# Kernel optimization log

Measured on AMD Instinct MI355X. Metric: run time of the kernel, lower is better.

Reference implementation:

```python
import jax, jax.numpy as jnp
import numpy as np

HIDDEN = 1024
N_EXPERTS = 8
TOP_K = 2
INTER = 1408
N_SHARED = 2
SCALE = 1.0  # routed_scaling_factor


def setup_inputs() -> dict:
    key = jax.random.key(0)
    ks = jax.random.split(key, 9)
    s_h = 1.0 / np.sqrt(HIDDEN)
    s_i = 1.0 / np.sqrt(INTER)
    x = jax.random.normal(ks[0], (2, 2048, HIDDEN), dtype=jnp.float32)
    gate_w = jax.random.uniform(ks[1], (N_EXPERTS, HIDDEN), jnp.float32, -s_h, s_h)  # kaiming_uniform-ish
    # routed experts: SwiGLU (gate, up, down), stacked over experts
    wg = jax.random.uniform(ks[2], (N_EXPERTS, HIDDEN, INTER), jnp.float32, -s_h, s_h)
    wu = jax.random.uniform(ks[3], (N_EXPERTS, HIDDEN, INTER), jnp.float32, -s_h, s_h)
    wd = jax.random.uniform(ks[4], (N_EXPERTS, INTER, HIDDEN), jnp.float32, -s_i, s_i)
    # shared experts: one SwiGLU with intermediate = INTER * N_SHARED
    si = INTER * N_SHARED
    s_si = 1.0 / np.sqrt(si)
    swg = jax.random.uniform(ks[5], (HIDDEN, si), jnp.float32, -s_h, s_h)
    swu = jax.random.uniform(ks[6], (HIDDEN, si), jnp.float32, -s_h, s_h)
    swd = jax.random.uniform(ks[7], (si, HIDDEN), jnp.float32, -s_si, s_si)
    return {"x": x, "gate_w": gate_w, "wg": wg, "wu": wu, "wd": wd,
            "swg": swg, "swu": swu, "swd": swd}


def reference(x, gate_w, wg, wu, wd, swg, swu, swd):
    B, S, H = x.shape
    xf = x.reshape(-1, H)                              # [T, H]
    T = xf.shape[0]
    # --- MoEGate (fp32) ---
    logits = xf.astype(jnp.float32) @ gate_w.astype(jnp.float32).T   # [T, E]
    scores = jax.nn.softmax(logits, axis=-1)
    topw, topi = jax.lax.top_k(scores, TOP_K)          # [T, K]
    denom = topw.sum(axis=-1, keepdims=True) + 1e-20   # norm_topk_prob (top_k > 1)
    topw = topw / denom * SCALE
    # dense combine weights [T, E]: zero except at top-k expert slots
    wdense = jnp.zeros((T, N_EXPERTS), jnp.float32).at[
        jnp.arange(T)[:, None], topi].set(topw)
    # --- routed experts (SwiGLU), computed densely per expert and combined ---
    hg = jnp.einsum('th,ehi->eti', xf, wg)             # [E, T, I]
    hu = jnp.einsum('th,ehi->eti', xf, wu)             # [E, T, I]
    eo = jnp.einsum('eti,eih->eth', jax.nn.silu(hg) * hu, wd)   # [E, T, H]
    y = jnp.einsum('te,eth->th', wdense, eo)           # weighted scatter-combine
    # --- shared experts ---
    shared = (jax.nn.silu(xf @ swg) * (xf @ swu)) @ swd
    return (y + shared).reshape(B, S, H)
```

## Files before the change

kernel.cpp:

```cpp
#include <hip/hip_runtime.h>
#include <hip/hip_bf16.h>
#include <math.h>

#define HIDDEN 1024
#define NEXP 8
#define TOPK 2
#define INTER 1408
#define SINTER 2816
#define NTOK 4096
#define NROWS (NTOK * TOPK)
#define NPANEL 10
#define TROWS 16384
#define MAXT 136

typedef unsigned short ushort_t;
typedef __attribute__((ext_vector_type(8))) short short8;
typedef __attribute__((ext_vector_type(4))) float f32x4;

__device__ __forceinline__ ushort_t f2bf(float f) {
    unsigned int b = __float_as_uint(f);
    unsigned int r = (b + 0x7FFFu + ((b >> 16) & 1u)) >> 16;
    return (ushort_t)r;
}
__device__ __forceinline__ float bf2f(ushort_t u) {
    return __uint_as_float(((unsigned int)u) << 16);
}
__device__ __forceinline__ float silu_f(float g) {
    return g * (1.0f / (1.0f + __expf(-g)));
}
__device__ __forceinline__ int imin(int a, int b) { return a < b ? a : b; }

#define GLDS16(gp, lp) __builtin_amdgcn_global_load_lds(                     \
    (const __attribute__((address_space(1))) void*)(gp),                     \
    (__attribute__((address_space(3))) void*)(lp), 16, 0, 0)

__global__ void conv_x(const float* __restrict__ src, ushort_t* __restrict__ dst) {
    int i = (blockIdx.x * 256 + threadIdx.x) * 4;
    float4 v = *reinterpret_cast<const float4*>(&src[i]);
    union { ushort_t h[4]; unsigned long long ll; } p;
    p.h[0] = f2bf(v.x); p.h[1] = f2bf(v.y); p.h[2] = f2bf(v.z); p.h[3] = f2bf(v.w);
    *reinterpret_cast<unsigned long long*>(&dst[i]) = p.ll;
}

__global__ __launch_bounds__(256) void tconv64(const float* __restrict__ src,
                                               ushort_t* __restrict__ dst,
                                               int R, int C, long sstride,
                                               long dstride) {
    src += (size_t)blockIdx.z * sstride;
    dst += (size_t)blockIdx.z * dstride;
    __shared__ float tile[32][65];
    int ct = blockIdx.x * 32, rt = blockIdx.y * 64;
    int j = threadIdx.x;
    {
        int r = j >> 2;
        int c0 = (j & 3) * 8;
        const float* s = &src[(size_t)(rt + r) * C + ct + c0];
        float4 v0 = *reinterpret_cast<const float4*>(s);
        float4 v1 = *reinterpret_cast<const float4*>(s + 4);
        tile[c0 + 0][r] = v0.x; tile[c0 + 1][r] = v0.y;
        tile[c0 + 2][r] = v0.z; tile[c0 + 3][r] = v0.w;
        tile[c0 + 4][r] = v1.x; tile[c0 + 5][r] = v1.y;
        tile[c0 + 6][r] = v1.z; tile[c0 + 7][r] = v1.w;
    }
    __syncthreads();
    {
        int c = j >> 3;
        int r0 = (j & 7) * 8;
        union { ushort_t h[8]; short8 v; } p;
#pragma unroll
        for (int i = 0; i < 8; i++) p.h[i] = f2bf(tile[c][r0 + i]);
        *reinterpret_cast<short8*>(&dst[(size_t)(ct + c) * R + rt + r0]) = p.v;
    }
}

__global__ void gate_kernel(const float* __restrict__ x, const float* __restrict__ gw,
                            int* __restrict__ top_i, float* __restrict__ top_w) {
    int t = blockIdx.x;
    int lane = threadIdx.x;
    const float* xr = x + (size_t)t * HIDDEN;
    float acc[NEXP];
#pragma unroll
    for (int e = 0; e < NEXP; e++) acc[e] = 0.f;
    for (int j = 0; j < HIDDEN / 64; j++) {
        float xv = xr[lane + 64 * j];
#pragma unroll
        for (int e = 0; e < NEXP; e++)
            acc[e] = fmaf(xv, gw[e * HIDDEN + lane + 64 * j], acc[e]);
    }
#pragma unroll
    for (int e = 0; e < NEXP; e++) {
        float v = acc[e];
        for (int off = 32; off > 0; off >>= 1) v += __shfl_xor(v, off, 64);
        acc[e] = v;
    }
    if (lane == 0) {
        float mx = acc[0];
        for (int e = 1; e < NEXP; e++) mx = fmaxf(mx, acc[e]);
        float s[NEXP];
        float sum = 0.f;
        for (int e = 0; e < NEXP; e++) { s[e] = __expf(acc[e] - mx); sum += s[e]; }
        float inv = 1.0f / sum;
        for (int e = 0; e < NEXP; e++) s[e] *= inv;
        int e0 = 0;
        for (int e = 1; e < NEXP; e++) if (s[e] > s[e0]) e0 = e;
        int e1 = -1;
        for (int e = 0; e < NEXP; e++) {
            if (e == e0) continue;
            if (e1 < 0 || s[e] > s[e1]) e1 = e;
        }
        float w0 = s[e0], w1 = s[e1];
        float denom = w0 + w1 + 1e-20f;
        top_i[t * 2 + 0] = e0;
        top_i[t * 2 + 1] = e1;
        top_w[t * 2 + 0] = w0 / denom;
        top_w[t * 2 + 1] = w1 / denom;
    }
}

__global__ void assign_kernel(const int* __restrict__ top_i, int* __restrict__ cnt,
                              int* __restrict__ rnk) {
    int j = blockIdx.x * blockDim.x + threadIdx.x;
    if (j < NROWS) rnk[j] = atomicAdd(&cnt[top_i[j]], 1);
}

__global__ void scan_kernel(const int* __restrict__ cnt, int* __restrict__ offs2,
                            int* __restrict__ cnt2, int* __restrict__ task_pm) {
    if (threadIdx.x == 0) {
        int o = 0;
        for (int e = 0; e < NEXP; e++) { offs2[e] = o; cnt2[e] = cnt[e]; o += cnt[e]; }
        offs2[8] = NROWS;          cnt2[8] = NTOK;
        offs2[9] = NROWS + NTOK;   cnt2[9] = NTOK;
        offs2[10] = TROWS;
        int t = 0;
        for (int e = 0; e < NPANEL; e++)
            for (int m0 = 0; m0 < cnt2[e]; m0 += 128)
                task_pm[t++] = (e << 16) | (m0 >> 7);
        for (; t < MAXT; t++) task_pm[t] = -1;
    }
}

__global__ void fill_kernel(const int* __restrict__ top_i, const float* __restrict__ top_w,
                            const int* __restrict__ rnk, const int* __restrict__ offs2,
                            int* __restrict__ tok_of_row, float* __restrict__ w_of_row,
                            int* __restrict__ inv_row) {
    int j = blockIdx.x * blockDim.x + threadIdx.x;
    if (j < NROWS) {
        int row = offs2[top_i[j]] + rnk[j];
        tok_of_row[row] = j;
        w_of_row[row] = top_w[j];
        inv_row[j] = row;
    }
}

__global__ void fill_shared(int* __restrict__ tok_of_row) {
    int j = blockIdx.x * blockDim.x + threadIdx.x;
    tok_of_row[NROWS + j] = (j & (NTOK - 1)) << 1;
}

__global__ __launch_bounds__(256, 2) void gemm_gu(
    const ushort_t* __restrict__ xb, const ushort_t* __restrict__ WgT,
    const ushort_t* __restrict__ WuT, ushort_t* __restrict__ act,
    const int* __restrict__ tok_of_row, const int* __restrict__ offs2,
    const int* __restrict__ cnt2, const int* __restrict__ task_pm) {
    int T = gridDim.x;
    int orig = blockIdx.x;
    int logical = (orig & 7) * (T >> 3) + (orig >> 3);
    int task = logical % MAXT;
    int nidx = logical / MAXT;
    int tk = task_pm[task];
    if (tk < 0) return;
    int e = tk >> 16;
    int m0 = (tk & 0xffff) << 7;
    int mcnt = cnt2[e];
    int base = offs2[e];
    int n0 = nidx * 128;
    const ushort_t* Bg = WgT + (size_t)e * INTER * HIDDEN;
    const ushort_t* Bu = WuT + (size_t)e * INTER * HIDDEN;

    __shared__ short As[8 * 1024];
    __shared__ short Bgs[8 * 1024];
    __shared__ short Bus[8 * 1024];

    int tid = threadIdx.x;
    int wave = tid >> 6, lane = tid & 63;
    int wr = wave >> 1, wc = wave & 1;
    int lr = lane & 15;
    int kq = (lane >> 4) * 8;

    int r0 = m0 + 32 * wave + lr, r1 = r0 + 16;
    int rr0 = base + imin(r0, mcnt - 1);
    int rr1 = base + imin(r1, mcnt - 1);
    const ushort_t* srcA0 = xb + (size_t)(tok_of_row[rr0] >> 1) * HIDDEN + kq;
    const ushort_t* srcA1 = xb + (size_t)(tok_of_row[rr1] >> 1) * HIDDEN + kq;
    const ushort_t* srcBg0 = Bg + (size_t)(n0 + 32 * wave + lr) * HIDDEN + kq;
    const ushort_t* srcBg1 = srcBg0 + (size_t)16 * HIDDEN;
    const ushort_t* srcBu0 = Bu + (size_t)(n0 + 32 * wave + lr) * HIDDEN + kq;
    const ushort_t* srcBu1 = srcBu0 + (size_t)16 * HIDDEN;

    f32x4 accG[4][4] = {};
    f32x4 accU[4][4] = {};

    for (int k0 = 0; k0 < HIDDEN; k0 += 64) {
        GLDS16(srcA0 + k0,      &As[(2 * wave) * 1024]);
        GLDS16(srcA0 + k0 + 32, &As[(2 * wave) * 1024 + 512]);
        GLDS16(srcA1 + k0,      &As[(2 * wave + 1) * 1024]);
        GLDS16(srcA1 + k0 + 32, &As[(2 * wave + 1) * 1024 + 512]);
        GLDS16(srcBg0 + k0,      &Bgs[(2 * wave) * 1024]);
        GLDS16(srcBg0 + k0 + 32, &Bgs[(2 * wave) * 1024 + 512]);
        GLDS16(srcBg1 + k0,      &Bgs[(2 * wave + 1) * 1024]);
        GLDS16(srcBg1 + k0 + 32, &Bgs[(2 * wave + 1) * 1024 + 512]);
        GLDS16(srcBu0 + k0,      &Bus[(2 * wave) * 1024]);
        GLDS16(srcBu0 + k0 + 32, &Bus[(2 * wave) * 1024 + 512]);
        GLDS16(srcBu1 + k0,      &Bus[(2 * wave + 1) * 1024]);
        GLDS16(srcBu1 + k0 + 32, &Bus[(2 * wave + 1) * 1024 + 512]);
        __syncthreads();
#pragma unroll
        for (int s = 0; s < 2; s++) {
            short8 a[4], bg[4], bu[4];
#pragma unroll
            for (int mi = 0; mi < 4; mi++)
                a[mi] = *reinterpret_cast<const short8*>(
                    &As[(wr * 4 + mi) * 1024 + s * 512 + lane * 8]);
#pragma unroll
            for (int ni = 0; ni < 4; ni++) {
                bg[ni] = *reinterpret_cast<const short8*>(
                    &Bgs[(wc * 4 + ni) * 1024 + s * 512 + lane * 8]);
                bu[ni] = *reinterpret_cast<const short8*>(
                    &Bus[(wc * 4 + ni) * 1024 + s * 512 + lane * 8]);
            }
#pragma unroll
            for (int mi = 0; mi < 4; mi++)
#pragma unroll
                for (int ni = 0; ni < 4; ni++) {
                    accG[mi][ni] = __builtin_amdgcn_mfma_f32_16x16x32_bf16(
                        a[mi], bg[ni], accG[mi][ni], 0, 0, 0);
                    accU[mi][ni] = __builtin_amdgcn_mfma_f32_16x16x32_bf16(
                        a[mi], bu[ni], accU[mi][ni], 0, 0, 0);
                }
        }
        __syncthreads();
    }

#pragma unroll
    for (int mi = 0; mi < 4; mi++) {
#pragma unroll
        for (int r = 0; r < 4; r++) {
            int gm = m0 + wr * 64 + mi * 16 + (lane >> 4) * 4 + r;
            if (gm < mcnt) {
#pragma unroll
                for (int ni = 0; ni < 4; ni++) {
                    int col = n0 + wc * 64 + ni * 16 + lr;
                    float g = accG[mi][ni][r], u = accU[mi][ni][r];
                    act[(size_t)(base + gm) * INTER + col] = f2bf(silu_f(g) * u);
                }
            }
        }
    }
}

__global__ __launch_bounds__(256, 2) void gemm_down(
    const ushort_t* __restrict__ act, const ushort_t* __restrict__ WdT,
    ushort_t* __restrict__ part, const int* __restrict__ offs2,
    const int* __restrict__ cnt2, const int* __restrict__ task_pm) {
    int T = gridDim.x;
    int orig = blockIdx.x;
    int logical = (orig & 7) * (T >> 3) + (orig >> 3);
    int task = logical % MAXT;
    int nidx = logical / MAXT;
    int tk = task_pm[task];
    if (tk < 0) return;
    int e = tk >> 16;
    int m0 = (tk & 0xffff) << 7;
    int mcnt = cnt2[e];
    int base = offs2[e];
    int n0 = nidx * 256;
    const ushort_t* Bd = WdT + (size_t)e * HIDDEN * INTER;

    __shared__ short As[8 * 1024];
    __shared__ short Bs[16 * 1024];

    int tid = threadIdx.x;
    int wave = tid >> 6, lane = tid & 63;
    int wr = wave >> 1, wc = wave & 1;
    int lr = lane & 15;
    int kq = (lane >> 4) * 8;

    const ushort_t* srcA0 = act + (size_t)(base + m0 + 32 * wave + lr) * INTER + kq;
    const ushort_t* srcA1 = srcA0 + (size_t)16 * INTER;
    const ushort_t* srcB0 = Bd + (size_t)(n0 + 64 * wave + lr) * INTER + kq;
    const ushort_t* srcB1 = srcB0 + (size_t)16 * INTER;
    const ushort_t* srcB2 = srcB0 + (size_t)32 * INTER;
    const ushort_t* srcB3 = srcB0 + (size_t)48 * INTER;

    f32x4 acc[4][8] = {};

    for (int k0 = 0; k0 < INTER; k0 += 64) {
        GLDS16(srcA0 + k0,      &As[(2 * wave) * 1024]);
        GLDS16(srcA0 + k0 + 32, &As[(2 * wave) * 1024 + 512]);
        GLDS16(srcA1 + k0,      &As[(2 * wave + 1) * 1024]);
        GLDS16(srcA1 + k0 + 32, &As[(2 * wave + 1) * 1024 + 512]);
        GLDS16(srcB0 + k0,      &Bs[(4 * wave) * 1024]);
        GLDS16(srcB0 + k0 + 32, &Bs[(4 * wave) * 1024 + 512]);
        GLDS16(srcB1 + k0,      &Bs[(4 * wave + 1) * 1024]);
        GLDS16(srcB1 + k0 + 32, &Bs[(4 * wave + 1) * 1024 + 512]);
        GLDS16(srcB2 + k0,      &Bs[(4 * wave + 2) * 1024]);
        GLDS16(srcB2 + k0 + 32, &Bs[(4 * wave + 2) * 1024 + 512]);
        GLDS16(srcB3 + k0,      &Bs[(4 * wave + 3) * 1024]);
        GLDS16(srcB3 + k0 + 32, &Bs[(4 * wave + 3) * 1024 + 512]);
        __syncthreads();
#pragma unroll
        for (int s = 0; s < 2; s++) {
            short8 a[4], b[8];
#pragma unroll
            for (int mi = 0; mi < 4; mi++)
                a[mi] = *reinterpret_cast<const short8*>(
                    &As[(wr * 4 + mi) * 1024 + s * 512 + lane * 8]);
#pragma unroll
            for (int ni = 0; ni < 8; ni++)
                b[ni] = *reinterpret_cast<const short8*>(
                    &Bs[(wc * 8 + ni) * 1024 + s * 512 + lane * 8]);
#pragma unroll
            for (int mi = 0; mi < 4; mi++)
#pragma unroll
                for (int ni = 0; ni < 8; ni++)
                    acc[mi][ni] = __builtin_amdgcn_mfma_f32_16x16x32_bf16(
                        a[mi], b[ni], acc[mi][ni], 0, 0, 0);
        }
        __syncthreads();
    }

#pragma unroll
    for (int mi = 0; mi < 4; mi++) {
#pragma unroll
        for (int r = 0; r < 4; r++) {
            int gm = m0 + wr * 64 + mi * 16 + (lane >> 4) * 4 + r;
            if (gm < mcnt) {
#pragma unroll
                for (int ni = 0; ni < 8; ni++) {
                    int col = n0 + wc * 128 + ni * 16 + lr;
                    part[(size_t)(base + gm) * HIDDEN + col] = f2bf(acc[mi][ni][r]);
                }
            }
        }
    }
}

__global__ __launch_bounds__(256) void combine_kernel(
    const ushort_t* __restrict__ part, const int* __restrict__ inv_row,
    const float* __restrict__ w_of_row, float* __restrict__ out) {
    int t = blockIdx.x;
    int c = threadIdx.x * 4;
    int r0 = inv_row[2 * t], r1 = inv_row[2 * t + 1];
    float w0 = w_of_row[r0], w1 = w_of_row[r1];
    ushort4 a0 = *reinterpret_cast<const ushort4*>(&part[(size_t)r0 * HIDDEN + c]);
    ushort4 a1 = *reinterpret_cast<const ushort4*>(&part[(size_t)r1 * HIDDEN + c]);
    ushort4 a2 = *reinterpret_cast<const ushort4*>(&part[((size_t)NROWS + t) * HIDDEN + c]);
    ushort4 a3 = *reinterpret_cast<const ushort4*>(&part[((size_t)NROWS + NTOK + t) * HIDDEN + c]);
    float4 o;
    o.x = w0 * bf2f(a0.x) + w1 * bf2f(a1.x) + bf2f(a2.x) + bf2f(a3.x);
    o.y = w0 * bf2f(a0.y) + w1 * bf2f(a1.y) + bf2f(a2.y) + bf2f(a3.y);
    o.z = w0 * bf2f(a0.z) + w1 * bf2f(a1.z) + bf2f(a2.z) + bf2f(a3.z);
    o.w = w0 * bf2f(a0.w) + w1 * bf2f(a1.w) + bf2f(a2.w) + bf2f(a3.w);
    *reinterpret_cast<float4*>(&out[(size_t)t * HIDDEN + c]) = o;
}

extern "C" void kernel_launch(void* const* d_in, const int* in_sizes, int n_in,
                              void* d_out, int out_size, void* d_ws, size_t ws_size,
                              hipStream_t stream) {
    const float* x   = (const float*)d_in[0];
    const float* gw  = (const float*)d_in[1];
    const float* wg  = (const float*)d_in[2];
    const float* wu  = (const float*)d_in[3];
    const float* wd  = (const float*)d_in[4];
    const float* swg = (const float*)d_in[5];
    const float* swu = (const float*)d_in[6];
    const float* swd = (const float*)d_in[7];
    float* out = (float*)d_out;

    const size_t XB   = (size_t)NTOK * HIDDEN;
    const size_t WPAN = (size_t)NPANEL * INTER * HIDDEN;
    const size_t ACT  = (size_t)TROWS * INTER;
    const size_t PART = (size_t)TROWS * HIDDEN;
    ushort_t* xb   = (ushort_t*)d_ws;
    ushort_t* wgT  = xb + XB;
    ushort_t* wuT  = wgT + WPAN;
    ushort_t* wdT  = wuT + WPAN;
    ushort_t* act  = wdT + WPAN;
    ushort_t* part = act + ACT;
    int* ib = (int*)(part + PART);
    int* top_i      = ib;
    int* rnk        = ib + NROWS;
    int* cnt        = ib + 2 * NROWS;
    int* offs2      = ib + 2 * NROWS + 8;
    int* cnt2       = offs2 + 16;
    int* task_pm    = cnt2 + 16;
    int* tok_of_row = task_pm + MAXT;
    int* inv_row    = tok_of_row + TROWS;
    float* top_w    = (float*)(inv_row + NROWS);
    float* w_of_row = top_w + NROWS;

    conv_x<<<(NTOK * HIDDEN) / (256 * 4), 256, 0, stream>>>(x, xb);
    tconv64<<<dim3(INTER / 32, HIDDEN / 64, NEXP), 256, 0, stream>>>(
        wg, wgT, HIDDEN, INTER, (long)HIDDEN * INTER, (long)INTER * HIDDEN);
    tconv64<<<dim3(INTER / 32, HIDDEN / 64, NEXP), 256, 0, stream>>>(
        wu, wuT, HIDDEN, INTER, (long)HIDDEN * INTER, (long)INTER * HIDDEN);
    tconv64<<<dim3(SINTER / 32, HIDDEN / 64, 1), 256, 0, stream>>>(
        swg, wgT + (size_t)8 * INTER * HIDDEN, HIDDEN, SINTER, 0, 0);
    tconv64<<<dim3(SINTER / 32, HIDDEN / 64, 1), 256, 0, stream>>>(
        swu, wuT + (size_t)8 * INTER * HIDDEN, HIDDEN, SINTER, 0, 0);
    tconv64<<<dim3(HIDDEN / 32, INTER / 64, NEXP), 256, 0, stream>>>(
        wd, wdT, INTER, HIDDEN, (long)INTER * HIDDEN, (long)HIDDEN * INTER);
    tconv64<<<dim3(HIDDEN / 32, INTER / 64, 2), 256, 0, stream>>>(
        swd, wdT + (size_t)8 * HIDDEN * INTER, INTER, HIDDEN,
        (long)INTER * HIDDEN, (long)HIDDEN * INTER);

    gate_kernel<<<NTOK, 64, 0, stream>>>(x, gw, top_i, top_w);
    hipMemsetAsync(cnt, 0, 8 * sizeof(int), stream);
    assign_kernel<<<NROWS / 256, 256, 0, stream>>>(top_i, cnt, rnk);
    scan_kernel<<<1, 1, 0, stream>>>(cnt, offs2, cnt2, task_pm);
    fill_kernel<<<NROWS / 256, 256, 0, stream>>>(top_i, top_w, rnk, offs2,
                                                 tok_of_row, w_of_row, inv_row);
    fill_shared<<<NROWS / 256, 256, 0, stream>>>(tok_of_row);

    gemm_gu<<<MAXT * (INTER / 128), 256, 0, stream>>>(
        xb, wgT, wuT, act, tok_of_row, offs2, cnt2, task_pm);
    gemm_down<<<MAXT * (HIDDEN / 256), 256, 0, stream>>>(
        act, wdT, part, offs2, cnt2, task_pm);
    combine_kernel<<<NTOK, 256, 0, stream>>>(part, inv_row, w_of_row, out);
}
```

Before: 390.4 us.

## Double-buffer LDS tiles in expert GEMMs to overlap loads with MFMA

```diff
diff --git a/kernel.cpp b/kernel.cpp
--- a/kernel.cpp
+++ b/kernel.cpp
@@ -177,9 +177,9 @@
     const ushort_t* Bg = WgT + (size_t)e * INTER * HIDDEN;
     const ushort_t* Bu = WuT + (size_t)e * INTER * HIDDEN;
 
-    __shared__ short As[8 * 1024];
-    __shared__ short Bgs[8 * 1024];
-    __shared__ short Bus[8 * 1024];
+    __shared__ short As[2][8 * 512];
+    __shared__ short Bgs[2][8 * 512];
+    __shared__ short Bus[2][8 * 512];
 
     int tid = threadIdx.x;
     int wave = tid >> 6, lane = tid & 63;
@@ -200,46 +200,49 @@
     f32x4 accG[4][4] = {};
     f32x4 accU[4][4] = {};
 
-    for (int k0 = 0; k0 < HIDDEN; k0 += 64) {
-        GLDS16(srcA0 + k0,      &As[(2 * wave) * 1024]);
-        GLDS16(srcA0 + k0 + 32, &As[(2 * wave) * 1024 + 512]);
-        GLDS16(srcA1 + k0,      &As[(2 * wave + 1) * 1024]);
-        GLDS16(srcA1 + k0 + 32, &As[(2 * wave + 1) * 1024 + 512]);
-        GLDS16(srcBg0 + k0,      &Bgs[(2 * wave) * 1024]);
-        GLDS16(srcBg0 + k0 + 32, &Bgs[(2 * wave) * 1024 + 512]);
-        GLDS16(srcBg1 + k0,      &Bgs[(2 * wave + 1) * 1024]);
-        GLDS16(srcBg1 + k0 + 32, &Bgs[(2 * wave + 1) * 1024 + 512]);
-        GLDS16(srcBu0 + k0,      &Bus[(2 * wave) * 1024]);
-        GLDS16(srcBu0 + k0 + 32, &Bus[(2 * wave) * 1024 + 512]);
-        GLDS16(srcBu1 + k0,      &Bus[(2 * wave + 1) * 1024]);
-        GLDS16(srcBu1 + k0 + 32, &Bus[(2 * wave + 1) * 1024 + 512]);
-        __syncthreads();
-#pragma unroll
-        for (int s = 0; s < 2; s++) {
-            short8 a[4], bg[4], bu[4];
-#pragma unroll
-            for (int mi = 0; mi < 4; mi++)
-                a[mi] = *reinterpret_cast<const short8*>(
-                    &As[(wr * 4 + mi) * 1024 + s * 512 + lane * 8]);
+#define STAGE_GU(buf, k0)                                                    \
+    do {                                                                     \
+        GLDS16(srcA0 + (k0), &As[buf][(2 * wave) * 512]);                    \
+        GLDS16(srcA1 + (k0), &As[buf][(2 * wave + 1) * 512]);                \
+        GLDS16(srcBg0 + (k0), &Bgs[buf][(2 * wave) * 512]);                  \
+        GLDS16(srcBg1 + (k0), &Bgs[buf][(2 * wave + 1) * 512]);              \
+        GLDS16(srcBu0 + (k0), &Bus[buf][(2 * wave) * 512]);                  \
+        GLDS16(srcBu1 + (k0), &Bus[buf][(2 * wave + 1) * 512]);              \
+    } while (0)
+
+    STAGE_GU(0, 0);
+    asm volatile("s_waitcnt vmcnt(0)" ::: "memory");
+    __builtin_amdgcn_s_barrier();
+
+    const int NT = HIDDEN / 32;
+    for (int t = 0; t < NT; t++) {
+        int cur = t & 1;
+        if (t + 1 < NT) STAGE_GU(cur ^ 1, (t + 1) * 32);
+        short8 a[4], bg[4], bu[4];
+#pragma unroll
+        for (int mi = 0; mi < 4; mi++)
+            a[mi] = *reinterpret_cast<const short8*>(
+                &As[cur][(wr * 4 + mi) * 512 + lane * 8]);
+#pragma unroll
+        for (int ni = 0; ni < 4; ni++) {
+            bg[ni] = *reinterpret_cast<const short8*>(
+                &Bgs[cur][(wc * 4 + ni) * 512 + lane * 8]);
+            bu[ni] = *reinterpret_cast<const short8*>(
+                &Bus[cur][(wc * 4 + ni) * 512 + lane * 8]);
+        }
+#pragma unroll
+        for (int mi = 0; mi < 4; mi++)
 #pragma unroll
             for (int ni = 0; ni < 4; ni++) {
-                bg[ni] = *reinterpret_cast<const short8*>(
-                    &Bgs[(wc * 4 + ni) * 1024 + s * 512 + lane * 8]);
-                bu[ni] = *reinterpret_cast<const short8*>(
-                    &Bus[(wc * 4 + ni) * 1024 + s * 512 + lane * 8]);
+                accG[mi][ni] = __builtin_amdgcn_mfma_f32_16x16x32_bf16(
+                    a[mi], bg[ni], accG[mi][ni], 0, 0, 0);
+                accU[mi][ni] = __builtin_amdgcn_mfma_f32_16x16x32_bf16(
+                    a[mi], bu[ni], accU[mi][ni], 0, 0, 0);
             }
-#pragma unroll
-            for (int mi = 0; mi < 4; mi++)
-#pragma unroll
-                for (int ni = 0; ni < 4; ni++) {
-                    accG[mi][ni] = __builtin_amdgcn_mfma_f32_16x16x32_bf16(
-                        a[mi], bg[ni], accG[mi][ni], 0, 0, 0);
-                    accU[mi][ni] = __builtin_amdgcn_mfma_f32_16x16x32_bf16(
-                        a[mi], bu[ni], accU[mi][ni], 0, 0, 0);
-                }
-        }
-        __syncthreads();
-    }
+        asm volatile("s_waitcnt vmcnt(0)" ::: "memory");
+        __builtin_amdgcn_s_barrier();
+    }
+#undef STAGE_GU
 
 #pragma unroll
     for (int mi = 0; mi < 4; mi++) {
@@ -276,8 +279,8 @@
     int n0 = nidx * 256;
     const ushort_t* Bd = WdT + (size_t)e * HIDDEN * INTER;
 
-    __shared__ short As[8 * 1024];
-    __shared__ short Bs[16 * 1024];
+    __shared__ short As[2][8 * 512];
+    __shared__ short Bs[2][16 * 512];
 
     int tid = threadIdx.x;
     int wave = tid >> 6, lane = tid & 63;
@@ -294,40 +297,43 @@
 
     f32x4 acc[4][8] = {};
 
-    for (int k0 = 0; k0 < INTER; k0 += 64) {
-        GLDS16(srcA0 + k0,      &As[(2 * wave) * 1024]);
-        GLDS16(srcA0 + k0 + 32, &As[(2 * wave) * 1024 + 512]);
-        GLDS16(srcA1 + k0,      &As[(2 * wave + 1) * 1024]);
-        GLDS16(srcA1 + k0 + 32, &As[(2 * wave + 1) * 1024 + 512]);
-        GLDS16(srcB0 + k0,      &Bs[(4 * wave) * 1024]);
-        GLDS16(srcB0 + k0 + 32, &Bs[(4 * wave) * 1024 + 512]);
-        GLDS16(srcB1 + k0,      &Bs[(4 * wave + 1) * 1024]);
-        GLDS16(srcB1 + k0 + 32, &Bs[(4 * wave + 1) * 1024 + 512]);
-        GLDS16(srcB2 + k0,      &Bs[(4 * wave + 2) * 1024]);
-        GLDS16(srcB2 + k0 + 32, &Bs[(4 * wave + 2) * 1024 + 512]);
-        GLDS16(srcB3 + k0,      &Bs[(4 * wave + 3) * 1024]);
-        GLDS16(srcB3 + k0 + 32, &Bs[(4 * wave + 3) * 1024 + 512]);
-        __syncthreads();
-#pragma unroll
-        for (int s = 0; s < 2; s++) {
-            short8 a[4], b[8];
-#pragma unroll
-            for (int mi = 0; mi < 4; mi++)
-                a[mi] = *reinterpret_cast<const short8*>(
-                    &As[(wr * 4 + mi) * 1024 + s * 512 + lane * 8]);
+#define STAGE_D(buf, k0)                                                     \
+    do {                                                                     \
+        GLDS16(srcA0 + (k0), &As[buf][(2 * wave) * 512]);                    \
+        GLDS16(srcA1 + (k0), &As[buf][(2 * wave + 1) * 512]);                \
+        GLDS16(srcB0 + (k0), &Bs[buf][(4 * wave) * 512]);                    \
+        GLDS16(srcB1 + (k0), &Bs[buf][(4 * wave + 1) * 512]);                \
+        GLDS16(srcB2 + (k0), &Bs[buf][(4 * wave + 2) * 512]);                \
+        GLDS16(srcB3 + (k0), &Bs[buf][(4 * wave + 3) * 512]);                \
+    } while (0)
+
+    STAGE_D(0, 0);
+    asm volatile("s_waitcnt vmcnt(0)" ::: "memory");
+    __builtin_amdgcn_s_barrier();
+
+    const int NT = INTER / 32;
+    for (int t = 0; t < NT; t++) {
+        int cur = t & 1;
+        if (t + 1 < NT) STAGE_D(cur ^ 1, (t + 1) * 32);
+        short8 a[4], b[8];
+#pragma unroll
+        for (int mi = 0; mi < 4; mi++)
+            a[mi] = *reinterpret_cast<const short8*>(
+                &As[cur][(wr * 4 + mi) * 512 + lane * 8]);
+#pragma unroll
+        for (int ni = 0; ni < 8; ni++)
+            b[ni] = *reinterpret_cast<const short8*>(
+                &Bs[cur][(wc * 8 + ni) * 512 + lane * 8]);
+#pragma unroll
+        for (int mi = 0; mi < 4; mi++)
 #pragma unroll
             for (int ni = 0; ni < 8; ni++)
-                b[ni] = *reinterpret_cast<const short8*>(
-                    &Bs[(wc * 8 + ni) * 1024 + s * 512 + lane * 8]);
-#pragma unroll
-            for (int mi = 0; mi < 4; mi++)
-#pragma unroll
-                for (int ni = 0; ni < 8; ni++)
-                    acc[mi][ni] = __builtin_amdgcn_mfma_f32_16x16x32_bf16(
-                        a[mi], b[ni], acc[mi][ni], 0, 0, 0);
-        }
-        __syncthreads();
-    }
+                acc[mi][ni] = __builtin_amdgcn_mfma_f32_16x16x32_bf16(
+                    a[mi], b[ni], acc[mi][ni], 0, 0, 0);
+        asm volatile("s_waitcnt vmcnt(0)" ::: "memory");
+        __builtin_amdgcn_s_barrier();
+    }
+#undef STAGE_D
 
 #pragma unroll
     for (int mi = 0; mi < 4; mi++) {
```

Measured after the change: 438.8 us. +12.4%, slower.

## Interleave gate/up weights into one panel and halve gate-up tile work

Applied to the files above, without the earlier changes.

```diff
diff --git a/kernel.cpp b/kernel.cpp
--- a/kernel.cpp
+++ b/kernel.cpp
@@ -12,6 +12,7 @@
 #define NPANEL 10
 #define TROWS 16384
 #define MAXT 136
+#define BPAN (SINTER * HIDDEN)
 
 typedef unsigned short ushort_t;
 typedef __attribute__((ext_vector_type(8))) short short8;
@@ -70,6 +71,41 @@
 #pragma unroll
         for (int i = 0; i < 8; i++) p.h[i] = f2bf(tile[c][r0 + i]);
         *reinterpret_cast<short8*>(&dst[(size_t)(ct + c) * R + rt + r0]) = p.v;
+    }
+}
+
+__global__ __launch_bounds__(256) void tconv64_gu(const float* __restrict__ src,
+                                                  ushort_t* __restrict__ dst,
+                                                  int C, long sstride,
+                                                  int base_panel, int goff) {
+    src += (size_t)blockIdx.z * sstride;
+    __shared__ float tile[32][65];
+    int ct = blockIdx.x * 32, rt = blockIdx.y * 64;
+    int j = threadIdx.x;
+    {
+        int r = j >> 2;
+        int c0 = (j & 3) * 8;
+        const float* s = &src[(size_t)(rt + r) * C + ct + c0];
+        float4 v0 = *reinterpret_cast<const float4*>(s);
+        float4 v1 = *reinterpret_cast<const float4*>(s + 4);
+        tile[c0 + 0][r] = v0.x; tile[c0 + 1][r] = v0.y;
+        tile[c0 + 2][r] = v0.z; tile[c0 + 3][r] = v0.w;
+        tile[c0 + 4][r] = v1.x; tile[c0 + 5][r] = v1.y;
+        tile[c0 + 6][r] = v1.z; tile[c0 + 7][r] = v1.w;
+    }
+    __syncthreads();
+    {
+        int c = j >> 3;
+        int r0 = (j & 7) * 8;
+        int gc = ct + c;
+        int panel = base_panel + blockIdx.z + gc / INTER;
+        int rl = gc % INTER;
+        int Rrow = ((rl >> 5) << 6) + (rl & 31) + goff;
+        union { ushort_t h[8]; short8 v; } p;
+#pragma unroll
+        for (int i = 0; i < 8; i++) p.h[i] = f2bf(tile[c][r0 + i]);
+        *reinterpret_cast<short8*>(
+            &dst[(size_t)panel * BPAN + (size_t)Rrow * HIDDEN + rt + r0]) = p.v;
     }
 }
 
@@ -157,11 +193,11 @@
     tok_of_row[NROWS + j] = (j & (NTOK - 1)) << 1;
 }
 
-__global__ __launch_bounds__(256, 2) void gemm_gu(
-    const ushort_t* __restrict__ xb, const ushort_t* __restrict__ WgT,
-    const ushort_t* __restrict__ WuT, ushort_t* __restrict__ act,
-    const int* __restrict__ tok_of_row, const int* __restrict__ offs2,
-    const int* __restrict__ cnt2, const int* __restrict__ task_pm) {
+__global__ __launch_bounds__(256, 4) void gemm_gu(
+    const ushort_t* __restrict__ xb, const ushort_t* __restrict__ Bhat,
+    ushort_t* __restrict__ act, const int* __restrict__ tok_of_row,
+    const int* __restrict__ offs2, const int* __restrict__ cnt2,
+    const int* __restrict__ task_pm) {
     int T = gridDim.x;
     int orig = blockIdx.x;
     int logical = (orig & 7) * (T >> 3) + (orig >> 3);
@@ -174,12 +210,10 @@
     int mcnt = cnt2[e];
     int base = offs2[e];
     int n0 = nidx * 128;
-    const ushort_t* Bg = WgT + (size_t)e * INTER * HIDDEN;
-    const ushort_t* Bu = WuT + (size_t)e * INTER * HIDDEN;
+    const ushort_t* B = Bhat + (size_t)e * BPAN;
 
     __shared__ short As[8 * 1024];
-    __shared__ short Bgs[8 * 1024];
-    __shared__ short Bus[8 * 1024];
+    __shared__ short Bs[8 * 1024];
 
     int tid = threadIdx.x;
     int wave = tid >> 6, lane = tid & 63;
@@ -192,55 +226,43 @@
     int rr1 = base + imin(r1, mcnt - 1);
     const ushort_t* srcA0 = xb + (size_t)(tok_of_row[rr0] >> 1) * HIDDEN + kq;
     const ushort_t* srcA1 = xb + (size_t)(tok_of_row[rr1] >> 1) * HIDDEN + kq;
-    const ushort_t* srcBg0 = Bg + (size_t)(n0 + 32 * wave + lr) * HIDDEN + kq;
-    const ushort_t* srcBg1 = srcBg0 + (size_t)16 * HIDDEN;
-    const ushort_t* srcBu0 = Bu + (size_t)(n0 + 32 * wave + lr) * HIDDEN + kq;
-    const ushort_t* srcBu1 = srcBu0 + (size_t)16 * HIDDEN;
-
-    f32x4 accG[4][4] = {};
-    f32x4 accU[4][4] = {};
+    const ushort_t* srcB0 = B + (size_t)(n0 + 32 * wave + lr) * HIDDEN + kq;
+    const ushort_t* srcB1 = srcB0 + (size_t)16 * HIDDEN;
+
+    f32x4 acc[4][4] = {};
 
     for (int k0 = 0; k0 < HIDDEN; k0 += 64) {
         GLDS16(srcA0 + k0,      &As[(2 * wave) * 1024]);
         GLDS16(srcA0 + k0 + 32, &As[(2 * wave) * 1024 + 512]);
         GLDS16(srcA1 + k0,      &As[(2 * wave + 1) * 1024]);
         GLDS16(srcA1 + k0 + 32, &As[(2 * wave + 1) * 1024 + 512]);
-        GLDS16(srcBg0 + k0,      &Bgs[(2 * wave) * 1024]);
-        GLDS16(srcBg0 + k0 + 32, &Bgs[(2 * wave) * 1024 + 512]);
-        GLDS16(srcBg1 + k0,      &Bgs[(2 * wave + 1) * 1024]);
-        GLDS16(srcBg1 + k0 + 32, &Bgs[(2 * wave + 1) * 1024 + 512]);
-        GLDS16(srcBu0 + k0,      &Bus[(2 * wave) * 1024]);
-        GLDS16(srcBu0 + k0 + 32, &Bus[(2 * wave) * 1024 + 512]);
-        GLDS16(srcBu1 + k0,      &Bus[(2 * wave + 1) * 1024]);
-        GLDS16(srcBu1 + k0 + 32, &Bus[(2 * wave + 1) * 1024 + 512]);
+        GLDS16(srcB0 + k0,      &Bs[(2 * wave) * 1024]);
+        GLDS16(srcB0 + k0 + 32, &Bs[(2 * wave) * 1024 + 512]);
+        GLDS16(srcB1 + k0,      &Bs[(2 * wave + 1) * 1024]);
+        GLDS16(srcB1 + k0 + 32, &Bs[(2 * wave + 1) * 1024 + 512]);
         __syncthreads();
 #pragma unroll
         for (int s = 0; s < 2; s++) {
-            short8 a[4], bg[4], bu[4];
+            short8 a[4], b[4];
 #pragma unroll
             for (int mi = 0; mi < 4; mi++)
                 a[mi] = *reinterpret_cast<const short8*>(
                     &As[(wr * 4 + mi) * 1024 + s * 512 + lane * 8]);
 #pragma unroll
-            for (int ni = 0; ni < 4; ni++) {
-                bg[ni] = *reinterpret_cast<const short8*>(
-                    &Bgs[(wc * 4 + ni) * 1024 + s * 512 + lane * 8]);
-                bu[ni] = *reinterpret_cast<const short8*>(
-                    &Bus[(wc * 4 + ni) * 1024 + s * 512 + lane * 8]);
-            }
+            for (int ni = 0; ni < 4; ni++)
+                b[ni] = *reinterpret_cast<const short8*>(
+                    &Bs[(wc * 4 + ni) * 1024 + s * 512 + lane * 8]);
 #pragma unroll
             for (int mi = 0; mi < 4; mi++)
 #pragma unroll
-                for (int ni = 0; ni < 4; ni++) {
-                    accG[mi][ni] = __builtin_amdgcn_mfma_f32_16x16x32_bf16(
-                        a[mi], bg[ni], accG[mi][ni], 0, 0, 0);
-                    accU[mi][ni] = __builtin_amdgcn_mfma_f32_16x16x32_bf16(
-                        a[mi], bu[ni], accU[mi][ni], 0, 0, 0);
-                }
+                for (int ni = 0; ni < 4; ni++)
+                    acc[mi][ni] = __builtin_amdgcn_mfma_f32_16x16x32_bf16(
+                        a[mi], b[ni], acc[mi][ni], 0, 0, 0);
         }
         __syncthreads();
     }
 
+    int colbase = 32 * ((n0 >> 6) + wc);
 #pragma unroll
     for (int mi = 0; mi < 4; mi++) {
 #pragma unroll
@@ -248,10 +270,10 @@
             int gm = m0 + wr * 64 + mi * 16 + (lane >> 4) * 4 + r;
             if (gm < mcnt) {
 #pragma unroll
-                for (int ni = 0; ni < 4; ni++) {
-                    int col = n0 + wc * 64 + ni * 16 + lr;
-                    float g = accG[mi][ni][r], u = accU[mi][ni][r];
-                    act[(size_t)(base + gm) * INTER + col] = f2bf(silu_f(g) * u);
+                for (int ni = 0; ni < 2; ni++) {
+                    float g = acc[mi][ni][r], u = acc[mi][ni + 2][r];
+                    act[(size_t)(base + gm) * INTER + colbase + ni * 16 + lr] =
+                        f2bf(silu_f(g) * u);
                 }
             }
         }
@@ -378,14 +400,14 @@
     float* out = (float*)d_out;
 
     const size_t XB   = (size_t)NTOK * HIDDEN;
-    const size_t WPAN = (size_t)NPANEL * INTER * HIDDEN;
+    const size_t BHAT = (size_t)NPANEL * BPAN;
+    const size_t WDT  = (size_t)NPANEL * INTER * HIDDEN;
     const size_t ACT  = (size_t)TROWS * INTER;
     const size_t PART = (size_t)TROWS * HIDDEN;
     ushort_t* xb   = (ushort_t*)d_ws;
-    ushort_t* wgT  = xb + XB;
-    ushort_t* wuT  = wgT + WPAN;
-    ushort_t* wdT  = wuT + WPAN;
-    ushort_t* act  = wdT + WPAN;
+    ushort_t* bhat = xb + XB;
+    ushort_t* wdT  = bhat + BHAT;
+    ushort_t* act  = wdT + WDT;
     ushort_t* part = act + ACT;
     int* ib = (int*)(part + PART);
     int* top_i      = ib;
@@ -400,14 +422,14 @@
     float* w_of_row = top_w + NROWS;
 
     conv_x<<<(NTOK * HIDDEN) / (256 * 4), 256, 0, stream>>>(x, xb);
-    tconv64<<<dim3(INTER / 32, HIDDEN / 64, NEXP), 256, 0, stream>>>(
-        wg, wgT, HIDDEN, INTER, (long)HIDDEN * INTER, (long)INTER * HIDDEN);
-    tconv64<<<dim3(INTER / 32, HIDDEN / 64, NEXP), 256, 0, stream>>>(
-        wu, wuT, HIDDEN, INTER, (long)HIDDEN * INTER, (long)INTER * HIDDEN);
-    tconv64<<<dim3(SINTER / 32, HIDDEN / 64, 1), 256, 0, stream>>>(
-        swg, wgT + (size_t)8 * INTER * HIDDEN, HIDDEN, SINTER, 0, 0);
-    tconv64<<<dim3(SINTER / 32, HIDDEN / 64, 1), 256, 0, stream>>>(
-        swu, wuT + (size_t)8 * INTER * HIDDEN, HIDDEN, SINTER, 0, 0);
+    tconv64_gu<<<dim3(INTER / 32, HIDDEN / 64, NEXP), 256, 0, stream>>>(
+        wg, bhat, INTER, (long)HIDDEN * INTER, 0, 0);
+    tconv64_gu<<<dim3(INTER / 32, HIDDEN / 64, NEXP), 256, 0, stream>>>(
+        wu, bhat, INTER, (long)HIDDEN * INTER, 0, 32);
+    tconv64_gu<<<dim3(SINTER / 32, HIDDEN / 64, 1), 256, 0, stream>>>(
+        swg, bhat, SINTER, 0, 8, 0);
+    tconv64_gu<<<dim3(SINTER / 32, HIDDEN / 64, 1), 256, 0, stream>>>(
+        swu, bhat, SINTER, 0, 8, 32);
     tconv64<<<dim3(HIDDEN / 32, INTER / 64, NEXP), 256, 0, stream>>>(
         wd, wdT, INTER, HIDDEN, (long)INTER * HIDDEN, (long)HIDDEN * INTER);
     tconv64<<<dim3(HIDDEN / 32, INTER / 64, 2), 256, 0, stream>>>(
@@ -422,8 +444,8 @@
                                                  tok_of_row, w_of_row, inv_row);
     fill_shared<<<NROWS / 256, 256, 0, stream>>>(tok_of_row);
 
-    gemm_gu<<<MAXT * (INTER / 128), 256, 0, stream>>>(
-        xb, wgT, wuT, act, tok_of_row, offs2, cnt2, task_pm);
+    gemm_gu<<<MAXT * (SINTER / 128), 256, 0, stream>>>(
+        xb, bhat, act, tok_of_row, offs2, cnt2, task_pm);
     gemm_down<<<MAXT * (HIDDEN / 256), 256, 0, stream>>>(
         act, wdT, part, offs2, cnt2, task_pm);
     combine_kernel<<<NTOK, 256, 0, stream>>>(part, inv_row, w_of_row, out);
```

Result: slower. 435.6 us (+11.6%).
